# Performance work log

Hardware: AMD Instinct MI355X
Metric: run time of the kernel (lower is better)

The kernel has to match this reference:

```python
import jax, jax.numpy as jnp
import numpy as np

B, E, H, T = 16384, 1024, 16, 256  # batch, embed_dim, num_heads, tabular_dim
HD = E // H  # head_dim


def _mha_seq1(q, kv, Wqkv, bqkv, Wo, bo):
    """nn.MultiheadAttention with query/key/value of seq_len 1 (batch_first).
    q, kv: [B, E]; Wqkv: [3E, E]; bqkv: [3E]; Wo: [E, E]; bo: [E]."""
    Wq, Wk, Wv = jnp.split(Wqkv, 3, axis=0)
    bq, bk, bv = jnp.split(bqkv, 3)
    qp = (q @ Wq.T + bq).reshape(-1, H, HD)   # [B, H, HD]
    kp = (kv @ Wk.T + bk).reshape(-1, H, HD)
    vp = (kv @ Wv.T + bv).reshape(-1, H, HD)
    scores = jnp.sum(qp * kp, axis=-1, keepdims=True) * (1.0 / HD ** 0.5)  # [B, H, 1]
    w = jax.nn.softmax(scores, axis=-1)       # softmax over 1 key -> all ones
    out = (w * vp).reshape(-1, E)             # [B, E]
    return out @ Wo.T + bo


def setup_inputs() -> dict:
    key = jax.random.key(0)
    ks = jax.random.split(key, 16)
    s_e = 1.0 / E ** 0.5
    s_t = 1.0 / T ** 0.5
    return {
        "text_features": jax.random.normal(ks[0], (B, E), jnp.float32),
        "ecg_features": jax.random.normal(ks[1], (B, E), jnp.float32),
        "tabular_features": jax.random.normal(ks[2], (B, T), jnp.float32),
        "Wc_text": jax.random.uniform(ks[3], (E, T), jnp.float32, -s_t, s_t),
        "bc_text": jax.random.uniform(ks[4], (E,), jnp.float32, -s_t, s_t),
        "Wc_ecg": jax.random.uniform(ks[5], (E, T), jnp.float32, -s_t, s_t),
        "bc_ecg": jax.random.uniform(ks[6], (E,), jnp.float32, -s_t, s_t),
        "Wqkv_a": jax.random.uniform(ks[7], (3 * E, E), jnp.float32, -s_e, s_e),
        "bqkv_a": jnp.zeros((3 * E,), jnp.float32),
        "Wo_a": jax.random.uniform(ks[8], (E, E), jnp.float32, -s_e, s_e),
        "bo_a": jnp.zeros((E,), jnp.float32),
        "Wqkv_b": jax.random.uniform(ks[9], (3 * E, E), jnp.float32, -s_e, s_e),
        "bqkv_b": jnp.zeros((3 * E,), jnp.float32),
        "Wo_b": jax.random.uniform(ks[10], (E, E), jnp.float32, -s_e, s_e),
        "bo_b": jnp.zeros((E,), jnp.float32),
    }


def reference(text_features, ecg_features, tabular_features,
              Wc_text, bc_text, Wc_ecg, bc_ecg,
              Wqkv_a, bqkv_a, Wo_a, bo_a,
              Wqkv_b, bqkv_b, Wo_b, bo_b):
    text_scale = jax.nn.sigmoid(tabular_features @ Wc_text.T + bc_text)
    ecg_scale = jax.nn.sigmoid(tabular_features @ Wc_ecg.T + bc_ecg)
    text_query = text_features * text_scale
    ecg_query = ecg_features * ecg_scale
    attn_a = _mha_seq1(text_query, ecg_features, Wqkv_a, bqkv_a, Wo_a, bo_a)
    attn_b = _mha_seq1(ecg_query, text_features, Wqkv_b, bqkv_b, Wo_b, bo_b)
    return jnp.concatenate([attn_a, attn_b], axis=-1)
```

## Files before the change

### kernel.cpp

```cpp
#include <hip/hip_runtime.h>
#include <hip/hip_bf16.h>
#include <stdint.h>

typedef __bf16 bf16_t;
typedef bf16_t bf16x8 __attribute__((ext_vector_type(8)));
typedef bf16_t bf16x4 __attribute__((ext_vector_type(4)));
typedef float  f32x4  __attribute__((ext_vector_type(4)));

#define E_DIM 1024
#define B_ROWS 16384

__device__ __forceinline__ void gload_lds16(const void* g, void* l) {
    __builtin_amdgcn_global_load_lds(
        (const __attribute__((address_space(1))) void*)g,
        (__attribute__((address_space(3))) void*)l,
        16, 0, 0);
}

__global__ __launch_bounds__(256) void prep_w_k(const float* __restrict__ Wqkv_a,
                                                const float* __restrict__ bqkv_a,
                                                const float* __restrict__ Wo_a,
                                                const float* __restrict__ bo_a,
                                                const float* __restrict__ Wqkv_b,
                                                const float* __restrict__ bqkv_b,
                                                const float* __restrict__ Wo_b,
                                                const float* __restrict__ bo_b,
                                                bf16_t* __restrict__ WoB,
                                                bf16_t* __restrict__ WvT,
                                                float* __restrict__ beff) {
    const size_t MAT = (size_t)E_DIM * E_DIM;
    __shared__ float t[64][65];
    int b = blockIdx.x;
    int tid = threadIdx.x;
    if (b < 2048) {
        const int n4 = (int)(MAT / 4);
        int i = b * 256 + tid;
        const float* src = (i < n4) ? Wo_a : Wo_b;
        int j = (i < n4) ? i : i - n4;
        f32x4 v = ((const f32x4*)src)[j];
        bf16x4 o;
        o[0] = (bf16_t)v[0]; o[1] = (bf16_t)v[1];
        o[2] = (bf16_t)v[2]; o[3] = (bf16_t)v[3];
        ((bf16x4*)WoB)[i] = o;
    } else if (b < 2560) {
        int x = b - 2048;
        int ms = x >> 8;
        const float* in = (ms ? Wqkv_b : Wqkv_a) + 2 * MAT;
        bf16_t* o = WvT + (size_t)ms * MAT;
        int bb = x & 255;
        int bx = bb & 15, by = bb >> 4;
        int j0 = by * 64, k0 = bx * 64;
#pragma unroll
        for (int p = 0; p < 4; ++p) {
            int u = tid + 256 * p;
            int r = u >> 4, c4 = u & 15;
            f32x4 v = *(const f32x4*)(in + (size_t)(j0 + r) * E_DIM + k0 + c4 * 4);
            t[r][c4 * 4 + 0] = v[0]; t[r][c4 * 4 + 1] = v[1];
            t[r][c4 * 4 + 2] = v[2]; t[r][c4 * 4 + 3] = v[3];
        }
        __syncthreads();
#pragma unroll
        for (int p = 0; p < 4; ++p) {
            int u = tid + 256 * p;
            int r = u >> 4, c4 = u & 15;
            bf16x4 ov;
            ov[0] = (bf16_t)t[c4 * 4 + 0][r];
            ov[1] = (bf16_t)t[c4 * 4 + 1][r];
            ov[2] = (bf16_t)t[c4 * 4 + 2][r];
            ov[3] = (bf16_t)t[c4 * 4 + 3][r];
            *(bf16x4*)(o + (size_t)(k0 + r) * E_DIM + j0 + c4 * 4) = ov;
        }
    } else {
        int idx = (b - 2560) * 4 + (tid >> 6);
        int lane = tid & 63;
        int sel = idx >> 10;
        int i = idx & 1023;
        const float* Wo = sel ? Wo_b : Wo_a;
        const float* bv = (sel ? bqkv_b : bqkv_a) + 2 * E_DIM;
        const float* bo = sel ? bo_b : bo_a;
        float s = 0.f;
        for (int j = lane; j < E_DIM; j += 64)
            s += Wo[(size_t)i * E_DIM + j] * bv[j];
#pragma unroll
        for (int o = 32; o > 0; o >>= 1) s += __shfl_down(s, o);
        if (lane == 0) beff[sel * E_DIM + i] = s + bo[i];
    }
}

__global__ __launch_bounds__(256, 2) void combo_k(const float* __restrict__ ecg,
                                                  const float* __restrict__ text,
                                                  bf16_t* __restrict__ Xb,
                                                  const bf16_t* __restrict__ WoB,
                                                  const bf16_t* __restrict__ WvT,
                                                  bf16_t* __restrict__ Weff) {
    const size_t MAT = (size_t)E_DIM * E_DIM;
    __shared__ __align__(16) bf16_t As[128][64];
    __shared__ __align__(16) bf16_t Bs[128][64];

    int b = blockIdx.x;
    int tid = threadIdx.x;

    if (b >= 128) {
        const int half = (B_ROWS * E_DIM) / 8;
        const int total = 2 * half;
        const int stride = 2048 * 256;
        for (int i = (b - 128) * 256 + tid; i < total; i += stride) {
            const float* src = (i < half) ? ecg : text;
            int j = (i < half) ? i : i - half;
            f32x4 lo = ((const f32x4*)src)[2 * j];
            f32x4 hi = ((const f32x4*)src)[2 * j + 1];
            bf16x8 v;
            v[0] = (bf16_t)lo[0]; v[1] = (bf16_t)lo[1]; v[2] = (bf16_t)lo[2]; v[3] = (bf16_t)lo[3];
            v[4] = (bf16_t)hi[0]; v[5] = (bf16_t)hi[1]; v[6] = (bf16_t)hi[2]; v[7] = (bf16_t)hi[3];
            ((bf16x8*)Xb)[i] = v;
        }
        return;
    }

    int bid = b;
    int ms = bid >> 6;
    int t  = bid & 63;
    int mt = t >> 3, nt = t & 7;
    const bf16_t* A  = WoB + (size_t)ms * MAT;
    const bf16_t* Bm = WvT + (size_t)ms * MAT;
    bf16_t*       C  = Weff + (size_t)ms * MAT;
    int m0 = mt * 128, n0 = nt * 128;

    int lane = tid & 63;
    int wid = tid >> 6;
    int wrow = (wid >> 1) * 64;
    int wcol = (wid & 1) * 64;
    int cl = lane & 15;
    int rg = lane >> 4;

    f32x4 acc[4][4] = {};

    for (int kt = 0; kt < 16; ++kt) {
#pragma unroll
        for (int i = 0; i < 4; ++i) {
            int chunk = i * 256 + wid * 64 + lane;
            int row = chunk >> 3;
            int kk8 = (chunk & 7) * 8;
            char* la = (char*)(&As[0][0]) + (size_t)(i * 256 + wid * 64) * 16;
            char* lb = (char*)(&Bs[0][0]) + (size_t)(i * 256 + wid * 64) * 16;
            gload_lds16(A  + (size_t)(m0 + row) * E_DIM + kt * 64 + kk8, la);
            gload_lds16(Bm + (size_t)(n0 + row) * E_DIM + kt * 64 + kk8, lb);
        }
        __syncthreads();
#pragma unroll
        for (int ks = 0; ks < 2; ++ks) {
            int kk = ks * 32 + rg * 8;
            bf16x8 af[4], bq[4];
#pragma unroll
            for (int m = 0; m < 4; ++m) af[m] = *(const bf16x8*)(&As[wrow + m * 16 + cl][kk]);
#pragma unroll
            for (int n = 0; n < 4; ++n) bq[n] = *(const bf16x8*)(&Bs[wcol + n * 16 + cl][kk]);
#pragma unroll
            for (int m = 0; m < 4; ++m)
#pragma unroll
                for (int n = 0; n < 4; ++n)
                    acc[m][n] = __builtin_amdgcn_mfma_f32_16x16x32_bf16(af[m], bq[n], acc[m][n], 0, 0, 0);
        }
        __syncthreads();
    }

#pragma unroll
    for (int m = 0; m < 4; ++m) {
        int r = m0 + wrow + m * 16 + rg * 4;
#pragma unroll
        for (int n = 0; n < 4; ++n) {
            int c = n0 + wcol + n * 16 + cl;
#pragma unroll
            for (int j = 0; j < 4; ++j)
                C[(size_t)(r + j) * E_DIM + c] = (bf16_t)acc[m][n][j];
        }
    }
}

#define VMW(n) asm volatile("s_waitcnt vmcnt(" #n ")" ::: "memory")
#define BAR()  __builtin_amdgcn_s_barrier()

__global__ __launch_bounds__(512, 2) void main_gemm_v2_k(const bf16_t* __restrict__ Xb,
                                                         const bf16_t* __restrict__ Weff,
                                                         const float* __restrict__ beff,
                                                         float* __restrict__ out) {
    const size_t MAT  = (size_t)E_DIM * E_DIM;
    const size_t XMAT = (size_t)B_ROWS * E_DIM;

    int bid = blockIdx.x;
    int wg = (bid & 7) * 64 + (bid >> 3);
    int nt = wg & 7;
    int mt = wg >> 3;
    int sel = nt >> 2;
    int n0 = (nt & 3) * 256;
    int m0 = mt * 256;

    const bf16_t* gA = Xb + (size_t)sel * XMAT + (size_t)m0 * E_DIM;
    const bf16_t* gB = Weff + (size_t)sel * MAT + (size_t)n0 * E_DIM;
    const float*  bb = beff + sel * E_DIM;

    __shared__ __align__(16) bf16_t sA[2][256 * 64];
    __shared__ __align__(16) bf16_t sB[2][256 * 64];

    int tid  = threadIdx.x;
    int lane = tid & 63;
    int wid  = tid >> 6;
    int wr = wid >> 1;
    int wc = wid & 1;
    int cl = lane & 15;
    int rg = lane >> 4;

    int c0 = tid, c1 = 512 + tid;
    int r0 = c0 >> 3, r1 = c1 >> 3;
    int go0 = r0 * E_DIM + (((c0 & 7) * 8) ^ ((r0 & 7) << 3));
    int go1 = r1 * E_DIM + (((c1 & 7) * 8) ^ ((r1 & 7) << 3));
    int ld0 = c0 * 8, ld1 = c1 * 8;

    int koff0 = (rg * 8) ^ ((cl & 7) << 3);
    int koff1 = (32 + rg * 8) ^ ((cl & 7) << 3);

    f32x4 acc[4][8] = {};
    bf16x8 af[4], bq[4];

#define STAGE_A(kt, h, prt) do { \
    gload_lds16(gA + (size_t)((h) * 128) * E_DIM + (kt) * 64 + go0, &sA[prt][(h) * 8192 + ld0]); \
    gload_lds16(gA + (size_t)((h) * 128) * E_DIM + (kt) * 64 + go1, &sA[prt][(h) * 8192 + ld1]); } while (0)
#define STAGE_B(kt, h, prt) do { \
    gload_lds16(gB + (size_t)((h) * 128) * E_DIM + (kt) * 64 + go0, &sB[prt][(h) * 8192 + ld0]); \
    gload_lds16(gB + (size_t)((h) * 128) * E_DIM + (kt) * 64 + go1, &sB[prt][(h) * 8192 + ld1]); } while (0)
#define RD_A(p, KOFF) do { _Pragma("unroll") for (int m = 0; m < 4; ++m) \
    af[m] = *(const bf16x8*)(&sA[p][(wr * 64 + m * 16 + cl) * 64 + (KOFF)]); } while (0)
#define RD_B(p, nh, KOFF) do { _Pragma("unroll") for (int n = 0; n < 4; ++n) \
    bq[n] = *(const bf16x8*)(&sB[p][((nh) * 128 + wc * 64 + n * 16 + cl) * 64 + (KOFF)]); } while (0)
#define MM(nh) do { __builtin_amdgcn_s_setprio(1); \
    _Pragma("unroll") for (int m = 0; m < 4; ++m) _Pragma("unroll") for (int n = 0; n < 4; ++n) \
        acc[m][(nh) * 4 + n] = __builtin_amdgcn_mfma_f32_16x16x32_bf16(af[m], bq[n], acc[m][(nh) * 4 + n], 0, 0, 0); \
    __builtin_amdgcn_s_setprio(0); } while (0)

    STAGE_A(0, 0, 0); STAGE_A(0, 1, 0); STAGE_B(0, 0, 0); STAGE_B(0, 1, 0);
    VMW(2);
    BAR();

#pragma unroll
    for (int t = 0; t < 16; ++t) {
        const int p = t & 1, pn = p ^ 1;
        RD_A(p, koff0); RD_B(p, 0, koff0);
        if (t < 15) { STAGE_A(t + 1, 0, pn); VMW(2); } else { VMW(0); }
        BAR();
        MM(0);
        BAR();
        RD_B(p, 1, koff0);
        if (t < 15) STAGE_A(t + 1, 1, pn);
        BAR();
        MM(1);
        BAR();
        RD_A(p, koff1); RD_B(p, 1, koff1);
        if (t < 15) STAGE_B(t + 1, 0, pn);
        BAR();
        MM(1);
        BAR();
        RD_B(p, 0, koff1);
        if (t < 15) { STAGE_B(t + 1, 1, pn); VMW(2); }
        BAR();
        MM(0);
        BAR();
    }

#pragma unroll
    for (int m = 0; m < 4; ++m) {
        int r = m0 + wr * 64 + m * 16 + rg * 4;
#pragma unroll
        for (int ni = 0; ni < 8; ++ni) {
            int ch = n0 + (ni >> 2) * 128 + wc * 64 + (ni & 3) * 16 + cl;
            float bias = bb[ch];
            size_t gc = (size_t)sel * E_DIM + ch;
#pragma unroll
            for (int j = 0; j < 4; ++j)
                out[(size_t)(r + j) * (2 * E_DIM) + gc] = acc[m][ni][j] + bias;
        }
    }
#undef STAGE_A
#undef STAGE_B
#undef RD_A
#undef RD_B
#undef MM
}

extern "C" void kernel_launch(void* const* d_in, const int* in_sizes, int n_in,
                              void* d_out, int out_size, void* d_ws, size_t ws_size,
                              hipStream_t stream) {
    const float* text   = (const float*)d_in[0];
    const float* ecg    = (const float*)d_in[1];
    const float* Wqkv_a = (const float*)d_in[7];
    const float* bqkv_a = (const float*)d_in[8];
    const float* Wo_a   = (const float*)d_in[9];
    const float* bo_a   = (const float*)d_in[10];
    const float* Wqkv_b = (const float*)d_in[11];
    const float* bqkv_b = (const float*)d_in[12];
    const float* Wo_b   = (const float*)d_in[13];
    const float* bo_b   = (const float*)d_in[14];

    const size_t MAT  = (size_t)E_DIM * E_DIM;
    const size_t XMAT = (size_t)B_ROWS * E_DIM;
    bf16_t* WoB  = (bf16_t*)d_ws;
    bf16_t* WvT  = WoB + 2 * MAT;
    bf16_t* Weff = WvT + 2 * MAT;
    float*  beff = (float*)(Weff + 2 * MAT);
    bf16_t* Xb   = (bf16_t*)(beff + 2 * E_DIM);

    prep_w_k<<<3072, 256, 0, stream>>>(Wqkv_a, bqkv_a, Wo_a, bo_a,
                                       Wqkv_b, bqkv_b, Wo_b, bo_b,
                                       WoB, WvT, beff);
    combo_k<<<2176, 256, 0, stream>>>(ecg, text, Xb, WoB, WvT, Weff);
    main_gemm_v2_k<<<512, 512, 0, stream>>>(Xb, Weff, beff, (float*)d_out);
}
```

Before: 135.4 us.

## Fuse fp32-to-bf16 activation conversion into main GEMM A-tile loads

```diff
diff --git a/kernel.cpp b/kernel.cpp
--- a/kernel.cpp
+++ b/kernel.cpp
@@ -87,39 +87,17 @@
     }
 }
 
-__global__ __launch_bounds__(256, 2) void combo_k(const float* __restrict__ ecg,
-                                                  const float* __restrict__ text,
-                                                  bf16_t* __restrict__ Xb,
-                                                  const bf16_t* __restrict__ WoB,
-                                                  const bf16_t* __restrict__ WvT,
-                                                  bf16_t* __restrict__ Weff) {
+__global__ __launch_bounds__(256, 2) void fuse_k(const bf16_t* __restrict__ WoB,
+                                                 const bf16_t* __restrict__ WvT,
+                                                 bf16_t* __restrict__ Weff) {
     const size_t MAT = (size_t)E_DIM * E_DIM;
     __shared__ __align__(16) bf16_t As[128][64];
     __shared__ __align__(16) bf16_t Bs[128][64];
 
     int b = blockIdx.x;
     int tid = threadIdx.x;
-
-    if (b >= 128) {
-        const int half = (B_ROWS * E_DIM) / 8;
-        const int total = 2 * half;
-        const int stride = 2048 * 256;
-        for (int i = (b - 128) * 256 + tid; i < total; i += stride) {
-            const float* src = (i < half) ? ecg : text;
-            int j = (i < half) ? i : i - half;
-            f32x4 lo = ((const f32x4*)src)[2 * j];
-            f32x4 hi = ((const f32x4*)src)[2 * j + 1];
-            bf16x8 v;
-            v[0] = (bf16_t)lo[0]; v[1] = (bf16_t)lo[1]; v[2] = (bf16_t)lo[2]; v[3] = (bf16_t)lo[3];
-            v[4] = (bf16_t)hi[0]; v[5] = (bf16_t)hi[1]; v[6] = (bf16_t)hi[2]; v[7] = (bf16_t)hi[3];
-            ((bf16x8*)Xb)[i] = v;
-        }
-        return;
-    }
-
-    int bid = b;
-    int ms = bid >> 6;
-    int t  = bid & 63;
+    int ms = b >> 6;
+    int t  = b & 63;
     int mt = t >> 3, nt = t & 7;
     const bf16_t* A  = WoB + (size_t)ms * MAT;
     const bf16_t* Bm = WvT + (size_t)ms * MAT;
@@ -180,89 +158,87 @@
 #define VMW(n) asm volatile("s_waitcnt vmcnt(" #n ")" ::: "memory")
 #define BAR()  __builtin_amdgcn_s_barrier()
 
-__global__ __launch_bounds__(512, 2) void main_gemm_v2_k(const bf16_t* __restrict__ Xb,
+__global__ __launch_bounds__(512, 2) void main_gemm_v5_k(const float* __restrict__ text,
+                                                         const float* __restrict__ ecg,
                                                          const bf16_t* __restrict__ Weff,
                                                          const float* __restrict__ beff,
                                                          float* __restrict__ out) {
-    const size_t MAT  = (size_t)E_DIM * E_DIM;
-    const size_t XMAT = (size_t)B_ROWS * E_DIM;
+    const size_t MAT = (size_t)E_DIM * E_DIM;
 
     int bid = blockIdx.x;
-    int wg = (bid & 7) * 64 + (bid >> 3);
+    int wg = (bid & 7) * 128 + (bid >> 3);
     int nt = wg & 7;
     int mt = wg >> 3;
     int sel = nt >> 2;
     int n0 = (nt & 3) * 256;
-    int m0 = mt * 256;
-
-    const bf16_t* gA = Xb + (size_t)sel * XMAT + (size_t)m0 * E_DIM;
+    int m0 = mt * 128;
+
+    const float*  gA = (sel ? text : ecg) + (size_t)m0 * E_DIM;
     const bf16_t* gB = Weff + (size_t)sel * MAT + (size_t)n0 * E_DIM;
     const float*  bb = beff + sel * E_DIM;
 
-    __shared__ __align__(16) bf16_t sA[2][256 * 64];
-    __shared__ __align__(16) bf16_t sB[2][256 * 64];
+    __shared__ __align__(16) float  sAf[2][8192];
+    __shared__ __align__(16) bf16_t sB[2][16384];
 
     int tid  = threadIdx.x;
     int lane = tid & 63;
     int wid  = tid >> 6;
-    int wr = wid >> 1;
-    int wc = wid & 1;
+    int wr = wid >> 2;
+    int wc = wid & 3;
     int cl = lane & 15;
     int rg = lane >> 4;
+    int c7 = cl & 7;
 
     int c0 = tid, c1 = 512 + tid;
     int r0 = c0 >> 3, r1 = c1 >> 3;
-    int go0 = r0 * E_DIM + (((c0 & 7) * 8) ^ ((r0 & 7) << 3));
-    int go1 = r1 * E_DIM + (((c1 & 7) * 8) ^ ((r1 & 7) << 3));
-    int ld0 = c0 * 8, ld1 = c1 * 8;
-
-    int koff0 = (rg * 8) ^ ((cl & 7) << 3);
-    int koff1 = (32 + rg * 8) ^ ((cl & 7) << 3);
-
-    f32x4 acc[4][8] = {};
+    int goA0 = r0 * E_DIM + (((c0 & 7) ^ (r0 & 7)) * 4);
+    int goA1 = r1 * E_DIM + (((c1 & 7) ^ (r1 & 7)) * 4);
+    int ldA0 = c0 * 4, ldA1 = c1 * 4;
+    int goB0 = r0 * E_DIM + (((c0 & 7) * 8) ^ ((r0 & 7) << 3));
+    int goB1 = r1 * E_DIM + (((c1 & 7) * 8) ^ ((r1 & 7) << 3));
+    int ldB0 = c0 * 8, ldB1 = c1 * 8;
+
+    f32x4 acc[4][4] = {};
     bf16x8 af[4], bq[4];
 
-#define STAGE_A(kt, h, prt) do { \
-    gload_lds16(gA + (size_t)((h) * 128) * E_DIM + (kt) * 64 + go0, &sA[prt][(h) * 8192 + ld0]); \
-    gload_lds16(gA + (size_t)((h) * 128) * E_DIM + (kt) * 64 + go1, &sA[prt][(h) * 8192 + ld1]); } while (0)
+#define STAGE_A(kt, kh, prt) do { \
+    gload_lds16(gA + (size_t)(kt) * 64 + (kh) * 32 + goA0, &sAf[prt][(kh) * 4096 + ldA0]); \
+    gload_lds16(gA + (size_t)(kt) * 64 + (kh) * 32 + goA1, &sAf[prt][(kh) * 4096 + ldA1]); } while (0)
 #define STAGE_B(kt, h, prt) do { \
-    gload_lds16(gB + (size_t)((h) * 128) * E_DIM + (kt) * 64 + go0, &sB[prt][(h) * 8192 + ld0]); \
-    gload_lds16(gB + (size_t)((h) * 128) * E_DIM + (kt) * 64 + go1, &sB[prt][(h) * 8192 + ld1]); } while (0)
-#define RD_A(p, KOFF) do { _Pragma("unroll") for (int m = 0; m < 4; ++m) \
-    af[m] = *(const bf16x8*)(&sA[p][(wr * 64 + m * 16 + cl) * 64 + (KOFF)]); } while (0)
-#define RD_B(p, nh, KOFF) do { _Pragma("unroll") for (int n = 0; n < 4; ++n) \
-    bq[n] = *(const bf16x8*)(&sB[p][((nh) * 128 + wc * 64 + n * 16 + cl) * 64 + (KOFF)]); } while (0)
-#define MM(nh) do { __builtin_amdgcn_s_setprio(1); \
+    gload_lds16(gB + (size_t)((h) * 128) * E_DIM + (kt) * 64 + goB0, &sB[prt][(h) * 8192 + ldB0]); \
+    gload_lds16(gB + (size_t)((h) * 128) * E_DIM + (kt) * 64 + goB1, &sB[prt][(h) * 8192 + ldB1]); } while (0)
+#define RD_A(p, kh) do { _Pragma("unroll") for (int m = 0; m < 4; ++m) { \
+    int R_ = wr * 64 + m * 16 + cl; \
+    f32x4 lo_ = *(const f32x4*)(&sAf[p][(kh) * 4096 + R_ * 32 + (((rg * 2) ^ c7) * 4)]); \
+    f32x4 hi_ = *(const f32x4*)(&sAf[p][(kh) * 4096 + R_ * 32 + (((rg * 2 + 1) ^ c7) * 4)]); \
+    bf16x8 v_; \
+    v_[0] = (bf16_t)lo_[0]; v_[1] = (bf16_t)lo_[1]; v_[2] = (bf16_t)lo_[2]; v_[3] = (bf16_t)lo_[3]; \
+    v_[4] = (bf16_t)hi_[0]; v_[5] = (bf16_t)hi_[1]; v_[6] = (bf16_t)hi_[2]; v_[7] = (bf16_t)hi_[3]; \
+    af[m] = v_; } } while (0)
+#define RD_B(p, kh) do { _Pragma("unroll") for (int n = 0; n < 4; ++n) \
+    bq[n] = *(const bf16x8*)(&sB[p][(wc * 64 + n * 16 + cl) * 64 + (((kh) * 32 + rg * 8) ^ (c7 << 3))]); } while (0)
+#define MM() do { __builtin_amdgcn_s_setprio(1); \
     _Pragma("unroll") for (int m = 0; m < 4; ++m) _Pragma("unroll") for (int n = 0; n < 4; ++n) \
-        acc[m][(nh) * 4 + n] = __builtin_amdgcn_mfma_f32_16x16x32_bf16(af[m], bq[n], acc[m][(nh) * 4 + n], 0, 0, 0); \
+        acc[m][n] = __builtin_amdgcn_mfma_f32_16x16x32_bf16(af[m], bq[n], acc[m][n], 0, 0, 0); \
     __builtin_amdgcn_s_setprio(0); } while (0)
 
-    STAGE_A(0, 0, 0); STAGE_A(0, 1, 0); STAGE_B(0, 0, 0); STAGE_B(0, 1, 0);
+    STAGE_A(0, 0, 0); STAGE_B(0, 0, 0); STAGE_B(0, 1, 0); STAGE_A(0, 1, 0);
     VMW(2);
     BAR();
 
 #pragma unroll
     for (int t = 0; t < 16; ++t) {
         const int p = t & 1, pn = p ^ 1;
-        RD_A(p, koff0); RD_B(p, 0, koff0);
-        if (t < 15) { STAGE_A(t + 1, 0, pn); VMW(2); } else { VMW(0); }
-        BAR();
-        MM(0);
-        BAR();
-        RD_B(p, 1, koff0);
-        if (t < 15) STAGE_A(t + 1, 1, pn);
-        BAR();
-        MM(1);
-        BAR();
-        RD_A(p, koff1); RD_B(p, 1, koff1);
-        if (t < 15) STAGE_B(t + 1, 0, pn);
-        BAR();
-        MM(1);
-        BAR();
-        RD_B(p, 0, koff1);
-        if (t < 15) { STAGE_B(t + 1, 1, pn); VMW(2); }
-        BAR();
-        MM(0);
+        RD_A(p, 0); RD_B(p, 0);
+        if (t < 15) { STAGE_A(t + 1, 0, pn); STAGE_B(t + 1, 0, pn); VMW(4); }
+        else        { VMW(0); }
+        BAR();
+        MM();
+        BAR();
+        RD_A(p, 1); RD_B(p, 1);
+        if (t < 15) { STAGE_B(t + 1, 1, pn); STAGE_A(t + 1, 1, pn); VMW(2); }
+        BAR();
+        MM();
         BAR();
     }
 
@@ -270,13 +246,13 @@
     for (int m = 0; m < 4; ++m) {
         int r = m0 + wr * 64 + m * 16 + rg * 4;
 #pragma unroll
-        for (int ni = 0; ni < 8; ++ni) {
-            int ch = n0 + (ni >> 2) * 128 + wc * 64 + (ni & 3) * 16 + cl;
+        for (int n = 0; n < 4; ++n) {
+            int ch = n0 + wc * 64 + n * 16 + cl;
             float bias = bb[ch];
             size_t gc = (size_t)sel * E_DIM + ch;
 #pragma unroll
             for (int j = 0; j < 4; ++j)
-                out[(size_t)(r + j) * (2 * E_DIM) + gc] = acc[m][ni][j] + bias;
+                out[(size_t)(r + j) * (2 * E_DIM) + gc] = acc[m][n][j] + bias;
         }
     }
 #undef STAGE_A
@@ -300,17 +276,15 @@
     const float* Wo_b   = (const float*)d_in[13];
     const float* bo_b   = (const float*)d_in[14];
 
-    const size_t MAT  = (size_t)E_DIM * E_DIM;
-    const size_t XMAT = (size_t)B_ROWS * E_DIM;
+    const size_t MAT = (size_t)E_DIM * E_DIM;
     bf16_t* WoB  = (bf16_t*)d_ws;
     bf16_t* WvT  = WoB + 2 * MAT;
     bf16_t* Weff = WvT + 2 * MAT;
     float*  beff = (float*)(Weff + 2 * MAT);
-    bf16_t* Xb   = (bf16_t*)(beff + 2 * E_DIM);
 
     prep_w_k<<<3072, 256, 0, stream>>>(Wqkv_a, bqkv_a, Wo_a, bo_a,
                                        Wqkv_b, bqkv_b, Wo_b, bo_b,
                                        WoB, WvT, beff);
-    combo_k<<<2176, 256, 0, stream>>>(ecg, text, Xb, WoB, WvT, Weff);
-    main_gemm_v2_k<<<512, 512, 0, stream>>>(Xb, Weff, beff, (float*)d_out);
-}
+    fuse_k<<<128, 256, 0, stream>>>(WoB, WvT, Weff);
+    main_gemm_v5_k<<<1024, 512, 0, stream>>>(text, ecg, Weff, beff, (float*)d_out);
+}
```

Result: slower. 199.6 us (+47.4%).
